# Performance work log

Hardware: AMD Instinct MI355X
Metric: run time of the kernel (lower is better)

The kernel has to match this reference:

```python
import jax, jax.numpy as jnp
import numpy as np


def setup_inputs() -> dict:
    key = jax.random.key(0)
    k1, k2 = jax.random.split(key)
    B, N, D = 4, 4096, 3
    set1 = jax.random.normal(k1, (B, N, D), dtype=jnp.float32)
    set2 = jax.random.normal(k2, (B, N, D), dtype=jnp.float32)
    return {"set1": set1, "set2": set2}


def reference(set1, set2):
    # set1: [B, N, d], set2: [B, M, d]
    # Pairwise Euclidean distances via the Gram-matrix identity
    x2 = jnp.sum(set1 * set1, axis=-1)                    # [B, N]
    y2 = jnp.sum(set2 * set2, axis=-1)                    # [B, M]
    xy = jnp.einsum('bnd,bmd->bnm', set1, set2)           # [B, N, M]
    d2 = jnp.maximum(x2[:, :, None] + y2[:, None, :] - 2.0 * xy, 0.0)
    dist = jnp.sqrt(d2)                                   # [B, N, M]
    term1 = jnp.mean(jnp.min(dist, axis=2), axis=1)       # mean over N of row mins
    term2 = jnp.mean(jnp.min(dist, axis=1), axis=1)       # mean over M of col mins
    # per-instance sum, then average over batch (matches ahd / instance_num)
    return jnp.mean(term1 + term2)
```

## Files before the change

### kernel.cpp

```cpp
#include <hip/hip_runtime.h>
#include <math.h>

#define BATCH 4
#define NPTS  4096
#define RPB   256
#define ROWS  4
#define ROWS_PER_BLOCK (RPB * ROWS)
#define CHUNKS (NPTS / ROWS_PER_BLOCK)
#define SEGS  32
#define SEG_LEN (NPTS / SEGS)

__global__ __launch_bounds__(RPB) void ahd_min_kernel(
    const float* __restrict__ set1, const float* __restrict__ set2,
    unsigned int* __restrict__ mins )
{
    const int dir      = blockIdx.z;
    const int b        = blockIdx.y;
    const int rowChunk = blockIdx.x / SEGS;
    const int seg      = blockIdx.x % SEGS;

    const float* __restrict__ X = dir ? set2 : set1;
    const float* __restrict__ Y = dir ? set1 : set2;

    __shared__ float4 ys[SEG_LEN];

    const float* ybase = Y + ((size_t)b * NPTS + (size_t)seg * SEG_LEN) * 3;
    for (int i = threadIdx.x; i < SEG_LEN; i += RPB) {
        const float y0 = ybase[i * 3 + 0];
        const float y1 = ybase[i * 3 + 1];
        const float y2 = ybase[i * 3 + 2];
        ys[i] = make_float4(y0, y1, y2, fmaf(y0, y0, fmaf(y1, y1, y2 * y2)));
    }
    __syncthreads();

    float nx0[ROWS], nx1[ROWS], nx2[ROWS], hx[ROWS], acc[ROWS];
    const int rowBase = rowChunk * ROWS_PER_BLOCK + threadIdx.x;
    #pragma unroll
    for (int r = 0; r < ROWS; ++r) {
        const float* xp = X + ((size_t)b * NPTS + rowBase + r * RPB) * 3;
        const float x0 = xp[0], x1 = xp[1], x2 = xp[2];
        nx0[r] = -2.0f * x0;
        nx1[r] = -2.0f * x1;
        nx2[r] = -2.0f * x2;
        hx[r]  = fmaf(x0, x0, fmaf(x1, x1, x2 * x2));
        acc[r] = 3.4e38f;
    }

    #pragma unroll 4
    for (int j = 0; j < SEG_LEN; ++j) {
        const float4 y = ys[j];
        #pragma unroll
        for (int r = 0; r < ROWS; ++r) {
            const float q = fmaf(nx0[r], y.x,
                            fmaf(nx1[r], y.y,
                            fmaf(nx2[r], y.z, y.w)));
            acc[r] = fminf(acc[r], q);
        }
    }

    unsigned int* base = mins + (size_t)dir * BATCH * NPTS + (size_t)b * NPTS;
    #pragma unroll
    for (int r = 0; r < ROWS; ++r) {
        const float d2 = fmaxf(acc[r] + hx[r], 0.0f);
        atomicMin(&base[rowBase + r * RPB], __float_as_uint(d2));
    }
}

__global__ __launch_bounds__(1024) void ahd_reduce_kernel(
    const unsigned int* __restrict__ mins, float* __restrict__ out)
{
    const int total4 = (2 * BATCH * NPTS) / 4;
    const uint4* m4 = (const uint4*)mins;
    float s = 0.f;
    for (int i = threadIdx.x; i < total4; i += 1024) {
        const uint4 v = m4[i];
        s += sqrtf(__uint_as_float(v.x)) + sqrtf(__uint_as_float(v.y))
           + sqrtf(__uint_as_float(v.z)) + sqrtf(__uint_as_float(v.w));
    }

    #pragma unroll
    for (int off = 32; off > 0; off >>= 1)
        s += __shfl_down(s, off, 64);

    __shared__ float ws[16];
    const int lane = threadIdx.x & 63;
    const int w    = threadIdx.x >> 6;
    if (lane == 0) ws[w] = s;
    __syncthreads();
    if (threadIdx.x < 16) {
        float t = ws[threadIdx.x];
        #pragma unroll
        for (int off = 8; off > 0; off >>= 1)
            t += __shfl_down(t, off, 64);
        if (threadIdx.x == 0)
            out[0] = t * (1.0f / (float)(BATCH * NPTS));
    }
}

extern "C" void kernel_launch(void* const* d_in, const int* in_sizes, int n_in,
                              void* d_out, int out_size, void* d_ws, size_t ws_size,
                              hipStream_t stream) {
    const float* set1 = (const float*)d_in[0];
    const float* set2 = (const float*)d_in[1];
    float* out = (float*)d_out;
    unsigned int* mins = (unsigned int*)d_ws;

    const size_t min_bytes = (size_t)2 * BATCH * NPTS * sizeof(unsigned int);
    hipMemsetAsync(mins, 0xFF, min_bytes, stream);

    dim3 grid(CHUNKS * SEGS, BATCH, 2);
    ahd_min_kernel<<<grid, dim3(RPB), 0, stream>>>(set1, set2, mins);
    ahd_reduce_kernel<<<1, dim3(1024), 0, stream>>>(mins, out);
}
```

Before: 27.33 us.

## Replace atomicMin and memset with per-segment partials and parallel fixed-point reduction

The min kernel now writes per-segment partial squared-distance minima to a workspace buffer instead of doing global atomicMin, which removes the memset launch. The reduce kernel becomes a 128-block kernel that takes the min over 32 segments, applies sqrt, and accumulates the sum through a 64-bit fixed-point atomicAdd. A last-block counter writes the final mean. The change trades one launch and atomic contention for about 4 MB of extra partial-buffer traffic, and it relies on the min kernel's first block resetting the counter and total before the reduce kernel runs.

```diff
diff --git a/kernel.cpp b/kernel.cpp
--- a/kernel.cpp
+++ b/kernel.cpp
@@ -10,10 +10,20 @@
 #define SEGS  32
 #define SEG_LEN (NPTS / SEGS)
 
+#define RED_BLOCKS 128
+#define FP_SCALE   268435456.0
+
+
 __global__ __launch_bounds__(RPB) void ahd_min_kernel(
     const float* __restrict__ set1, const float* __restrict__ set2,
-    unsigned int* __restrict__ mins )
+    float* __restrict__ part, unsigned long long* __restrict__ total,
+    unsigned int* __restrict__ counter)
 {
+    if (blockIdx.x == 0 && blockIdx.y == 0 && blockIdx.z == 0 && threadIdx.x == 0) {
+        *total = 0ULL;
+        *counter = 0u;
+    }
+
     const int dir      = blockIdx.z;
     const int b        = blockIdx.y;
     const int rowChunk = blockIdx.x / SEGS;
@@ -58,42 +68,49 @@
         }
     }
 
-    unsigned int* base = mins + (size_t)dir * BATCH * NPTS + (size_t)b * NPTS;
+    float* dst = part + (((size_t)(dir * BATCH + b) * SEGS + seg) * NPTS);
     #pragma unroll
-    for (int r = 0; r < ROWS; ++r) {
-        const float d2 = fmaxf(acc[r] + hx[r], 0.0f);
-        atomicMin(&base[rowBase + r * RPB], __float_as_uint(d2));
-    }
+    for (int r = 0; r < ROWS; ++r)
+        dst[rowBase + r * RPB] = fmaxf(acc[r] + hx[r], 0.0f);
 }
 
-__global__ __launch_bounds__(1024) void ahd_reduce_kernel(
-    const unsigned int* __restrict__ mins, float* __restrict__ out)
+__global__ __launch_bounds__(RPB) void ahd_reduce_kernel(
+    const float* __restrict__ part, unsigned long long* __restrict__ total,
+    unsigned int* __restrict__ counter, float* __restrict__ out)
 {
-    const int total4 = (2 * BATCH * NPTS) / 4;
-    const uint4* m4 = (const uint4*)mins;
-    float s = 0.f;
-    for (int i = threadIdx.x; i < total4; i += 1024) {
-        const uint4 v = m4[i];
-        s += sqrtf(__uint_as_float(v.x)) + sqrtf(__uint_as_float(v.y))
-           + sqrtf(__uint_as_float(v.z)) + sqrtf(__uint_as_float(v.w));
-    }
+    const int g    = blockIdx.x * RPB + threadIdx.x;
+    const int dirb = g >> 12;
+    const int n    = g & (NPTS - 1);
+
+    const float* p = part + ((size_t)dirb * SEGS) * NPTS + n;
+    float m = p[0];
+    #pragma unroll
+    for (int s = 1; s < SEGS; ++s)
+        m = fminf(m, p[(size_t)s * NPTS]);
+
+    float d = sqrtf(m);
 
     #pragma unroll
     for (int off = 32; off > 0; off >>= 1)
-        s += __shfl_down(s, off, 64);
+        d += __shfl_down(d, off, 64);
 
-    __shared__ float ws[16];
+    __shared__ unsigned long long ws[4];
     const int lane = threadIdx.x & 63;
     const int w    = threadIdx.x >> 6;
-    if (lane == 0) ws[w] = s;
+    if (lane == 0)
+        ws[w] = (unsigned long long)((double)d * FP_SCALE);
     __syncthreads();
-    if (threadIdx.x < 16) {
-        float t = ws[threadIdx.x];
-        #pragma unroll
-        for (int off = 8; off > 0; off >>= 1)
-            t += __shfl_down(t, off, 64);
-        if (threadIdx.x == 0)
-            out[0] = t * (1.0f / (float)(BATCH * NPTS));
+
+    if (threadIdx.x == 0) {
+        const unsigned long long bs = ws[0] + ws[1] + ws[2] + ws[3];
+        atomicAdd(total, bs);
+        __threadfence();
+        const unsigned int cnt = atomicAdd(counter, 1u);
+        if (cnt == (unsigned int)(gridDim.x - 1)) {
+            const unsigned long long fin = atomicAdd(total, 0ULL);
+            out[0] = (float)((double)fin * (1.0 / FP_SCALE)
+                             * (1.0 / (double)(BATCH * NPTS)));
+        }
     }
 }
 
@@ -103,12 +120,12 @@
     const float* set1 = (const float*)d_in[0];
     const float* set2 = (const float*)d_in[1];
     float* out = (float*)d_out;
-    unsigned int* mins = (unsigned int*)d_ws;
 
-    const size_t min_bytes = (size_t)2 * BATCH * NPTS * sizeof(unsigned int);
-    hipMemsetAsync(mins, 0xFF, min_bytes, stream);
+    unsigned long long* total = (unsigned long long*)d_ws;
+    unsigned int* counter = (unsigned int*)((char*)d_ws + 8);
+    float* part = (float*)((char*)d_ws + 64);
 
     dim3 grid(CHUNKS * SEGS, BATCH, 2);
-    ahd_min_kernel<<<grid, dim3(RPB), 0, stream>>>(set1, set2, mins);
-    ahd_reduce_kernel<<<1, dim3(1024), 0, stream>>>(mins, out);
+    ahd_min_kernel<<<grid, dim3(RPB), 0, stream>>>(set1, set2, part, total, counter);
+    ahd_reduce_kernel<<<RED_BLOCKS, dim3(RPB), 0, stream>>>(part, total, counter, out);
 }
```

Result: faster. 24.65 us (-9.8%).
